# Performance work log

Hardware: AMD Instinct MI355X
Metric: run time of the kernel (lower is better)

The kernel has to match this reference:

```python
import jax, jax.numpy as jnp
import numpy as np
from jax import lax

B, V, N = 32, 3, 128          # batch, views, worm points
H, W = 512, 512               # image_size
DECAY_FACTOR = 10.0           # MAX_DECAY_FACTOR buffer value
OOB = 1e-05                   # oob_grad_val
MAX_STEPS = 10
LR, ALPHA, EPS = 0.2, 0.99, 1e-08  # torch.optim.RMSprop defaults (lr=0.2)

_b = jnp.arange(B)[:, None, None]   # (B,1,1)
_c = jnp.arange(V)[None, :, None]   # (1,3,1)


def _get_yx(p):
    # round -> long -> clamp to [0, H-1]; col 1 is y (row), col 0 is x (col)
    pi = jnp.clip(jnp.round(p).astype(jnp.int32), 0, H - 1)
    return pi[..., 1], pi[..., 0]  # each (B,3,N)


def _points_to_masks(p):
    y, x = _get_yx(p)
    return jnp.zeros((B, V, H, W), jnp.float32).at[_b, _c, y, x].set(1.0)


def _gradient_surface(masks_diff):
    grad0 = -masks_diff  # (B,3,H,W)
    grads = [grad0]
    g = grad0
    while g.shape[-1] > 1:
        gp = jnp.pad(g, ((0, 0), (0, 0), (1, 1), (1, 1)), constant_values=OOB)
        g = lax.reduce_window(gp, 0.0, lax.add, (1, 1, 3, 3), (1, 1, 2, 2), 'VALID') / 9.0
        grads.append(g)
    gs = jnp.zeros_like(grad0)
    for g in grads:
        # F.interpolate bilinear align_corners=False == jax.image.resize 'linear'
        gs = gs + jax.image.resize(g, grad0.shape, 'linear')
    ga = gs / len(grads)
    gapx = jnp.pad(ga, ((0, 0), (0, 0), (1, 1), (0, 0)), mode='edge')
    gx = (gapx[:, :, :-2] - gapx[:, :, 2:]) * 0.5   # central diff along H
    gapy = jnp.pad(ga, ((0, 0), (0, 0), (0, 0), (1, 1)), mode='edge')
    gy = (gapy[..., :-2] - gapy[..., 2:]) * 0.5     # central diff along W
    return jnp.stack([gx, gy])  # (2,B,3,H,W)


def setup_inputs() -> dict:
    key = jax.random.key(0)
    k1, k2 = jax.random.split(key)
    points_2d = jax.random.uniform(k1, (B, V, N, 2), jnp.float32) * (H - 1)
    masks_target = jax.random.uniform(k2, (B, V, H, W), jnp.float32)
    return {'points_2d': points_2d, 'masks_target': masks_target}


def reference(points_2d, masks_target):
    decay = jnp.exp(-jnp.arange(N, dtype=jnp.float32) / N * DECAY_FACTOR)  # (N,)
    masks_out = _points_to_masks(points_2d)
    masks_diff = masks_target - 0.01 * masks_out
    J = _gradient_surface(masks_diff)  # (2,B,3,H,W)
    p0 = lax.stop_gradient(points_2d)  # matches .clone().detach()

    def body(carry, _):
        p, sq, done = carry
        y, x = _get_yx(p)
        pl = (1.0 - masks_target[_b, _c, y, x]) * decay  # (B,3,N)
        cont = pl.max() > 0.1
        active = jnp.logical_and(jnp.logical_not(done), cont)
        gxp = J[0][_b, _c, y, x]
        gyp = J[1][_b, _c, y, x]
        g = -jnp.stack([gyp, gxp], axis=-1) * pl[..., None]  # (B,3,N,2)
        # RMSprop step
        sq_n = ALPHA * sq + (1.0 - ALPHA) * g * g
        p_n = p - LR * g / (jnp.sqrt(sq_n) + EPS)
        p = jnp.where(active, p_n, p)
        sq = jnp.where(active, sq_n, sq)
        done = jnp.logical_or(done, jnp.logical_not(cont))
        return (p, sq, done), None

    (p_opt, _, _), _ = lax.scan(body, (p0, jnp.zeros_like(p0), jnp.array(False)), None, length=MAX_STEPS)
    masks_opt = _points_to_masks(p_opt)
    return masks_out, masks_opt, p_opt
```

## Files before the change

kernel.cpp:

```cpp
#include <hip/hip_runtime.h>

#define IMGS 96
#define HW   262144
#define NPTS 12288
#define OOBV 1e-5f

static constexpr size_t PYR_OFF   = 0;
static constexpr size_t P_OFF     = 8388576;
static constexpr size_t SQ_OFF    = 8413152;
static constexpr size_t PLMAX_OFF = 8437728;
static constexpr size_t CNT_OFF   = 8437739;
static constexpr size_t LIST_OFF  = 8437740;
static constexpr size_t GA_OFF    = 8450560;

__device__ __forceinline__ int clampi(int v, int lo, int hi) {
    v = v < lo ? lo : v;
    return v > hi ? hi : v;
}

__global__ void k_scatter_init(const float* __restrict__ pts, const float* __restrict__ mt,
                               float* __restrict__ mo, int* __restrict__ cnt,
                               int* __restrict__ plist, float* __restrict__ p,
                               float* __restrict__ sq, float* __restrict__ plmax) {
    int i = blockIdx.x * blockDim.x + threadIdx.x;
    if (i >= NPTS) return;
    float px = pts[2*i], py = pts[2*i+1];
    int xi = clampi((int)rintf(px), 0, 511);
    int yi = clampi((int)rintf(py), 0, 511);
    int img = i >> 7, n = i & 127;
    int gp = img * HW + yi * 512 + xi;
    float old = atomicExch(&mo[gp], 1.0f);
    if (old == 0.0f) {
        int k = atomicAdd(cnt, 1);
        plist[k] = gp;
    }
    p[2*i] = px; p[2*i+1] = py;
    sq[2*i] = 0.0f; sq[2*i+1] = 0.0f;
    float d = expf(-(float)n * 0.078125f);
    float pl = (1.0f - mt[(size_t)img * HW + yi*512 + xi]) * d;
    atomicMax((int*)plmax, __float_as_int(pl));
}

__global__ void k_lvl1(const float* __restrict__ mt, float* __restrict__ out) {
    int t = blockIdx.x * blockDim.x + threadIdx.x;
    if (t >= IMGS * 65536) return;
    int j = t & 255, i = (t >> 8) & 255, img = t >> 16;
    const float* m = mt + (size_t)img * HW;
    float s = 0.0f;
    #pragma unroll
    for (int dy = -1; dy <= 1; ++dy) {
        int y = 2*i + dy;
        #pragma unroll
        for (int dx = -1; dx <= 1; ++dx) {
            int x = 2*j + dx;
            s += (y >= 0 && y < 512 && x >= 0 && x < 512) ? -m[y*512 + x] : OOBV;
        }
    }
    out[t] = s / 9.0f;
}

__global__ void k_corr1(const int* __restrict__ cnt, const int* __restrict__ plist,
                        float* __restrict__ lvl1) {
    int k = blockIdx.x * blockDim.x + threadIdx.x;
    if (k >= *cnt) return;
    int gp = plist[k];
    int img = gp >> 18;
    int r = gp & (HW - 1);
    int y = r >> 9, x = r & 511;
    float* L = lvl1 + (size_t)img * 65536;
    const float c = 0.01f / 9.0f;
    int ilo = y >> 1, ihi = ((y + 1) >> 1) > 255 ? 255 : ((y + 1) >> 1);
    int jlo = x >> 1, jhi = ((x + 1) >> 1) > 255 ? 255 : ((x + 1) >> 1);
    for (int i = ilo; i <= ihi; ++i)
        for (int j = jlo; j <= jhi; ++j)
            atomicAdd(&L[i*256 + j], c);
}

__global__ void k_lvl2(const float* __restrict__ in, float* __restrict__ out) {
    int t = blockIdx.x * blockDim.x + threadIdx.x;
    if (t >= IMGS * 16384) return;
    int j = t & 127, i = (t >> 7) & 127, img = t >> 14;
    const float* m = in + (size_t)img * 65536;
    float s = 0.0f;
    #pragma unroll
    for (int dy = -1; dy <= 1; ++dy) {
        int y = 2*i + dy;
        #pragma unroll
        for (int dx = -1; dx <= 1; ++dx) {
            int x = 2*j + dx;
            s += (y >= 0 && y < 256 && x >= 0 && x < 256) ? m[y*256 + x] : OOBV;
        }
    }
    out[t] = s / 9.0f;
}

__global__ __launch_bounds__(256) void k_pyrtail(float* __restrict__ pyr) {
    __shared__ float buf[5461];
    int img = blockIdx.x;
    const float* L2 = pyr + 6291456 + (size_t)img * 16384;
    for (int t = threadIdx.x; t < 4096; t += 256) {
        int i = t >> 6, j = t & 63;
        float s = 0.0f;
        #pragma unroll
        for (int dy = -1; dy <= 1; ++dy) {
            int y = 2*i + dy;
            #pragma unroll
            for (int dx = -1; dx <= 1; ++dx) {
                int x = 2*j + dx;
                s += (y >= 0 && y < 128 && x >= 0 && x < 128) ? L2[y*128 + x] : OOBV;
            }
        }
        float v = s / 9.0f;
        buf[t] = v;
        pyr[7864320 + (size_t)img * 4096 + t] = v;
    }
    __syncthreads();
    int inOff = 0, sin = 64;
    size_t goff = 8257536;
    while (sin > 1) {
        int sout = sin >> 1;
        int outOff = inOff + sin * sin;
        for (int t = threadIdx.x; t < sout * sout; t += 256) {
            int i = t / sout, j = t - i * sout;
            float s = 0.0f;
            for (int dy = -1; dy <= 1; ++dy) {
                int y = 2*i + dy;
                for (int dx = -1; dx <= 1; ++dx) {
                    int x = 2*j + dx;
                    s += (y >= 0 && y < sin && x >= 0 && x < sin) ? buf[inOff + y*sin + x] : OOBV;
                }
            }
            float v = s / 9.0f;
            buf[outOff + t] = v;
            pyr[goff + (size_t)img * sout * sout + t] = v;
        }
        __syncthreads();
        inOff = outOff; sin = sout;
        goff += (size_t)96 * sout * sout;
    }
}

__global__ __launch_bounds__(256) void k_ga(const float* __restrict__ mt,
                                            const float* __restrict__ pyr,
                                            float* __restrict__ ga) {
    __shared__ float vrow[520];
    int img = blockIdx.x >> 9;
    int h = blockIdx.x & 511;
    float hf = (float)h;

    for (int e = threadIdx.x; e < 520; e += 256) {
        int l = 0, rem = e;
        while (true) {
            int len = (256 >> l) + 1;
            if (rem < len) break;
            rem -= len; ++l;
        }
        int s = 256 >> l;
        int x = rem < s ? rem : s - 1;
        float scale = (float)s * (1.0f / 512.0f);
        float fy = (hf + 0.5f) * scale - 0.5f;
        fy = fminf(fmaxf(fy, 0.0f), (float)(s - 1));
        float fyf = floorf(fy);
        int y0 = (int)fyf;
        float ty = fy - fyf;
        int yb = (y0 + 1 < s) ? y0 + 1 : s - 1;
        const float* Lp = pyr + (8388608 - (8388608 >> (2*l))) + (size_t)img * s * s;
        float a = Lp[y0*s + x], b = Lp[yb*s + x];
        vrow[e] = (1.0f - ty) * a + ty * b;
    }
    __syncthreads();

    #pragma unroll
    for (int rep = 0; rep < 2; ++rep) {
        int w = threadIdx.x + rep * 256;
        int idx = img * HW + h * 512 + w;
        float wf = (float)w;
        float acc = -mt[idx];
        #pragma unroll
        for (int l = 0; l < 9; ++l) {
            const int s = 256 >> l;
            const float scale = (float)s * (1.0f / 512.0f);
            float fx = (wf + 0.5f) * scale - 0.5f;
            fx = fminf(fmaxf(fx, 0.0f), (float)(s - 1));
            float fxf = floorf(fx);
            int x0 = (int)fxf;
            float tx = fx - fxf;
            const int vo = 512 - (512 >> l) + l;
            float a = vrow[vo + x0], b = vrow[vo + x0 + 1];
            acc += (1.0f - tx) * a + tx * b;
        }
        ga[idx] = acc / 10.0f;
    }
}

__global__ void k_corrga(const int* __restrict__ cnt, const int* __restrict__ plist,
                         float* __restrict__ ga) {
    int k = blockIdx.x * blockDim.x + threadIdx.x;
    if (k >= *cnt) return;
    ga[plist[k]] += 0.001f;
}

__global__ void k_step(const float* __restrict__ mt, const float* __restrict__ ga,
                       float* __restrict__ p, float* __restrict__ sq,
                       float* __restrict__ plmax, int t) {
    int i = blockIdx.x * blockDim.x + threadIdx.x;
    if (i >= NPTS) return;
    float plm = plmax[t];
    if (!(plm > 0.1f)) {
        if (i == 0) plmax[t+1] = plm;
        return;
    }
    float px = p[2*i], py = p[2*i+1];
    int xi = clampi((int)rintf(px), 0, 511);
    int yi = clampi((int)rintf(py), 0, 511);
    int img = i >> 7, n = i & 127;
    const float* M = mt + (size_t)img * HW;
    const float* G = ga + (size_t)img * HW;
    float d = expf(-(float)n * 0.078125f);
    float pl = (1.0f - M[yi*512 + xi]) * d;
    float gxp = (G[clampi(yi-1,0,511)*512 + xi] - G[clampi(yi+1,0,511)*512 + xi]) * 0.5f;
    float gyp = (G[yi*512 + clampi(xi-1,0,511)] - G[yi*512 + clampi(xi+1,0,511)]) * 0.5f;
    float g0 = -gyp * pl;
    float g1 = -gxp * pl;
    float s0 = 0.99f * sq[2*i]   + 0.01f * g0 * g0;
    float s1 = 0.99f * sq[2*i+1] + 0.01f * g1 * g1;
    float p0 = px - 0.2f * g0 / (sqrtf(s0) + 1e-8f);
    float p1 = py - 0.2f * g1 / (sqrtf(s1) + 1e-8f);
    p[2*i] = p0; p[2*i+1] = p1;
    sq[2*i] = s0; sq[2*i+1] = s1;
    int xi2 = clampi((int)rintf(p0), 0, 511);
    int yi2 = clampi((int)rintf(p1), 0, 511);
    float pl2 = (1.0f - M[yi2*512 + xi2]) * d;
    atomicMax((int*)(plmax + t + 1), __float_as_int(pl2));
}

__global__ void k_final(const float* __restrict__ p, float* __restrict__ mopt,
                        float* __restrict__ pout) {
    int i = blockIdx.x * blockDim.x + threadIdx.x;
    if (i >= NPTS) return;
    float px = p[2*i], py = p[2*i+1];
    pout[2*i] = px; pout[2*i+1] = py;
    int xi = clampi((int)rintf(px), 0, 511);
    int yi = clampi((int)rintf(py), 0, 511);
    mopt[(i >> 7) * HW + yi*512 + xi] = 1.0f;
}

extern "C" void kernel_launch(void* const* d_in, const int* in_sizes, int n_in,
                              void* d_out, int out_size, void* d_ws, size_t ws_size,
                              hipStream_t stream) {
    const float* pts = (const float*)d_in[0];
    const float* mt  = (const float*)d_in[1];
    if (in_sizes[0] != NPTS * 2) { const float* tmp = pts; pts = mt; mt = tmp; }

    float* out  = (float*)d_out;
    float* mo   = out;
    float* mopt = out + (size_t)IMGS * HW;
    float* pout = out + 2 * (size_t)IMGS * HW;

    float* ws    = (float*)d_ws;
    float* pyr   = ws + PYR_OFF;
    float* p     = ws + P_OFF;
    float* sq    = ws + SQ_OFF;
    float* plmax = ws + PLMAX_OFF;
    int*   cnt   = (int*)(ws + CNT_OFF);
    int*   plist = (int*)(ws + LIST_OFF);
    float* ga    = ws + GA_OFF;

    hipMemsetAsync(out, 0, (size_t)out_size * sizeof(float), stream);
    hipMemsetAsync(plmax, 0, 12 * sizeof(float), stream);

    k_scatter_init<<<NPTS/256, 256, 0, stream>>>(pts, mt, mo, cnt, plist, p, sq, plmax);
    k_lvl1<<<IMGS*65536/256, 256, 0, stream>>>(mt, pyr);
    k_corr1<<<NPTS/256, 256, 0, stream>>>(cnt, plist, pyr);
    k_lvl2<<<IMGS*16384/256, 256, 0, stream>>>(pyr, pyr + 6291456);
    k_pyrtail<<<IMGS, 256, 0, stream>>>(pyr);
    k_ga<<<IMGS*512, 256, 0, stream>>>(mt, pyr, ga);
    k_corrga<<<NPTS/256, 256, 0, stream>>>(cnt, plist, ga);
    for (int t = 0; t < 10; ++t)
        k_step<<<NPTS/256, 256, 0, stream>>>(mt, ga, p, sq, plmax, t);
    k_final<<<NPTS/256, 256, 0, stream>>>(p, mopt, pout);
}
```

Measured before the change: 482.8 us.

## Run all RMSprop steps in one speculative kernel with a conditional fixup pass

Replaces ten per-step launches with a single kernel that runs every point through all ten RMSprop steps in registers. It records the per-step max loss with wave-level shuffle reductions and atomics. A second kernel reads the recorded maxima and, only if early stopping should have triggered, recomputes each point's trajectory up to the stop step. This removes the per-step launch overhead and the global p/sq traffic, at the cost of a redundant recomputation when the stop condition fires.

```diff
diff --git a/kernel.cpp b/kernel.cpp
--- a/kernel.cpp
+++ b/kernel.cpp
@@ -6,39 +6,30 @@
 #define OOBV 1e-5f
 
 static constexpr size_t PYR_OFF   = 0;
-static constexpr size_t P_OFF     = 8388576;
-static constexpr size_t SQ_OFF    = 8413152;
-static constexpr size_t PLMAX_OFF = 8437728;
-static constexpr size_t CNT_OFF   = 8437739;
-static constexpr size_t LIST_OFF  = 8437740;
-static constexpr size_t GA_OFF    = 8450560;
+static constexpr size_t PFIN_OFF  = 8388576;
+static constexpr size_t PLMAX_OFF = 8413152;
+static constexpr size_t CNT_OFF   = 8413163;
+static constexpr size_t LIST_OFF  = 8413164;
+static constexpr size_t GA_OFF    = 8425472;
 
 __device__ __forceinline__ int clampi(int v, int lo, int hi) {
     v = v < lo ? lo : v;
     return v > hi ? hi : v;
 }
 
-__global__ void k_scatter_init(const float* __restrict__ pts, const float* __restrict__ mt,
-                               float* __restrict__ mo, int* __restrict__ cnt,
-                               int* __restrict__ plist, float* __restrict__ p,
-                               float* __restrict__ sq, float* __restrict__ plmax) {
+__global__ void k_scatter(const float* __restrict__ pts, float* __restrict__ mo,
+                          int* __restrict__ cnt, int* __restrict__ plist) {
     int i = blockIdx.x * blockDim.x + threadIdx.x;
     if (i >= NPTS) return;
     float px = pts[2*i], py = pts[2*i+1];
     int xi = clampi((int)rintf(px), 0, 511);
     int yi = clampi((int)rintf(py), 0, 511);
-    int img = i >> 7, n = i & 127;
-    int gp = img * HW + yi * 512 + xi;
+    int gp = (i >> 7) * HW + yi * 512 + xi;
     float old = atomicExch(&mo[gp], 1.0f);
     if (old == 0.0f) {
         int k = atomicAdd(cnt, 1);
         plist[k] = gp;
     }
-    p[2*i] = px; p[2*i+1] = py;
-    sq[2*i] = 0.0f; sq[2*i+1] = 0.0f;
-    float d = expf(-(float)n * 0.078125f);
-    float pl = (1.0f - mt[(size_t)img * HW + yi*512 + xi]) * d;
-    atomicMax((int*)plmax, __float_as_int(pl));
 }
 
 __global__ void k_lvl1(const float* __restrict__ mt, float* __restrict__ out) {
@@ -200,38 +191,71 @@
     ga[plist[k]] += 0.001f;
 }
 
-__global__ void k_step(const float* __restrict__ mt, const float* __restrict__ ga,
-                       float* __restrict__ p, float* __restrict__ sq,
-                       float* __restrict__ plmax, int t) {
-    int i = blockIdx.x * blockDim.x + threadIdx.x;
-    if (i >= NPTS) return;
-    float plm = plmax[t];
-    if (!(plm > 0.1f)) {
-        if (i == 0) plmax[t+1] = plm;
-        return;
-    }
-    float px = p[2*i], py = p[2*i+1];
-    int xi = clampi((int)rintf(px), 0, 511);
-    int yi = clampi((int)rintf(py), 0, 511);
+__global__ __launch_bounds__(256) void k_traj(const float* __restrict__ pts,
+                                              const float* __restrict__ mt,
+                                              const float* __restrict__ ga,
+                                              float* __restrict__ pfin,
+                                              float* __restrict__ plmax) {
+    int i = blockIdx.x * 256 + threadIdx.x;
+    float px = pts[2*i], py = pts[2*i+1];
     int img = i >> 7, n = i & 127;
     const float* M = mt + (size_t)img * HW;
     const float* G = ga + (size_t)img * HW;
     float d = expf(-(float)n * 0.078125f);
-    float pl = (1.0f - M[yi*512 + xi]) * d;
-    float gxp = (G[clampi(yi-1,0,511)*512 + xi] - G[clampi(yi+1,0,511)*512 + xi]) * 0.5f;
-    float gyp = (G[yi*512 + clampi(xi-1,0,511)] - G[yi*512 + clampi(xi+1,0,511)]) * 0.5f;
-    float g0 = -gyp * pl;
-    float g1 = -gxp * pl;
-    float s0 = 0.99f * sq[2*i]   + 0.01f * g0 * g0;
-    float s1 = 0.99f * sq[2*i+1] + 0.01f * g1 * g1;
-    float p0 = px - 0.2f * g0 / (sqrtf(s0) + 1e-8f);
-    float p1 = py - 0.2f * g1 / (sqrtf(s1) + 1e-8f);
-    p[2*i] = p0; p[2*i+1] = p1;
-    sq[2*i] = s0; sq[2*i+1] = s1;
-    int xi2 = clampi((int)rintf(p0), 0, 511);
-    int yi2 = clampi((int)rintf(p1), 0, 511);
-    float pl2 = (1.0f - M[yi2*512 + xi2]) * d;
-    atomicMax((int*)(plmax + t + 1), __float_as_int(pl2));
+    float s0 = 0.0f, s1 = 0.0f;
+
+    for (int t = 0; t < 10; ++t) {
+        int xi = clampi((int)rintf(px), 0, 511);
+        int yi = clampi((int)rintf(py), 0, 511);
+        float pl = (1.0f - M[yi*512 + xi]) * d;
+        float r = pl;
+        #pragma unroll
+        for (int off = 32; off; off >>= 1) r = fmaxf(r, __shfl_xor(r, off, 64));
+        if ((threadIdx.x & 63) == 0)
+            atomicMax((int*)&plmax[t], __float_as_int(r));
+        float gxp = (G[clampi(yi-1,0,511)*512 + xi] - G[clampi(yi+1,0,511)*512 + xi]) * 0.5f;
+        float gyp = (G[yi*512 + clampi(xi-1,0,511)] - G[yi*512 + clampi(xi+1,0,511)]) * 0.5f;
+        float g0 = -gyp * pl;
+        float g1 = -gxp * pl;
+        s0 = 0.99f * s0 + 0.01f * g0 * g0;
+        s1 = 0.99f * s1 + 0.01f * g1 * g1;
+        px = px - 0.2f * g0 / (sqrtf(s0) + 1e-8f);
+        py = py - 0.2f * g1 / (sqrtf(s1) + 1e-8f);
+    }
+    pfin[2*i] = px; pfin[2*i+1] = py;
+}
+
+__global__ __launch_bounds__(256) void k_fix(const float* __restrict__ pts,
+                                             const float* __restrict__ mt,
+                                             const float* __restrict__ ga,
+                                             float* __restrict__ pfin,
+                                             const float* __restrict__ plmax) {
+    int tstop = 10;
+    for (int t = 0; t < 10; ++t) {
+        if (!(plmax[t] > 0.1f)) { tstop = t; break; }
+    }
+    if (tstop == 10) return;
+    int i = blockIdx.x * 256 + threadIdx.x;
+    float px = pts[2*i], py = pts[2*i+1];
+    int img = i >> 7, n = i & 127;
+    const float* M = mt + (size_t)img * HW;
+    const float* G = ga + (size_t)img * HW;
+    float d = expf(-(float)n * 0.078125f);
+    float s0 = 0.0f, s1 = 0.0f;
+    for (int t = 0; t < tstop; ++t) {
+        int xi = clampi((int)rintf(px), 0, 511);
+        int yi = clampi((int)rintf(py), 0, 511);
+        float pl = (1.0f - M[yi*512 + xi]) * d;
+        float gxp = (G[clampi(yi-1,0,511)*512 + xi] - G[clampi(yi+1,0,511)*512 + xi]) * 0.5f;
+        float gyp = (G[yi*512 + clampi(xi-1,0,511)] - G[yi*512 + clampi(xi+1,0,511)]) * 0.5f;
+        float g0 = -gyp * pl;
+        float g1 = -gxp * pl;
+        s0 = 0.99f * s0 + 0.01f * g0 * g0;
+        s1 = 0.99f * s1 + 0.01f * g1 * g1;
+        px = px - 0.2f * g0 / (sqrtf(s0) + 1e-8f);
+        py = py - 0.2f * g1 / (sqrtf(s1) + 1e-8f);
+    }
+    pfin[2*i] = px; pfin[2*i+1] = py;
 }
 
 __global__ void k_final(const float* __restrict__ p, float* __restrict__ mopt,
@@ -259,8 +283,7 @@
 
     float* ws    = (float*)d_ws;
     float* pyr   = ws + PYR_OFF;
-    float* p     = ws + P_OFF;
-    float* sq    = ws + SQ_OFF;
+    float* pfin  = ws + PFIN_OFF;
     float* plmax = ws + PLMAX_OFF;
     int*   cnt   = (int*)(ws + CNT_OFF);
     int*   plist = (int*)(ws + LIST_OFF);
@@ -269,14 +292,14 @@
     hipMemsetAsync(out, 0, (size_t)out_size * sizeof(float), stream);
     hipMemsetAsync(plmax, 0, 12 * sizeof(float), stream);
 
-    k_scatter_init<<<NPTS/256, 256, 0, stream>>>(pts, mt, mo, cnt, plist, p, sq, plmax);
+    k_scatter<<<NPTS/256, 256, 0, stream>>>(pts, mo, cnt, plist);
     k_lvl1<<<IMGS*65536/256, 256, 0, stream>>>(mt, pyr);
     k_corr1<<<NPTS/256, 256, 0, stream>>>(cnt, plist, pyr);
     k_lvl2<<<IMGS*16384/256, 256, 0, stream>>>(pyr, pyr + 6291456);
     k_pyrtail<<<IMGS, 256, 0, stream>>>(pyr);
     k_ga<<<IMGS*512, 256, 0, stream>>>(mt, pyr, ga);
     k_corrga<<<NPTS/256, 256, 0, stream>>>(cnt, plist, ga);
-    for (int t = 0; t < 10; ++t)
-        k_step<<<NPTS/256, 256, 0, stream>>>(mt, ga, p, sq, plmax, t);
-    k_final<<<NPTS/256, 256, 0, stream>>>(p, mopt, pout);
-}
+    k_traj<<<NPTS/256, 256, 0, stream>>>(pts, mt, ga, pfin, plmax);
+    k_fix<<<NPTS/256, 256, 0, stream>>>(pts, mt, ga, pfin, plmax);
+    k_final<<<NPTS/256, 256, 0, stream>>>(pfin, mopt, pout);
+}
```

Result: faster. 433.5 us (-10.2%).
